# Optimization experiments

Hardware: AMD Instinct MI355X
Metric: run time of the kernel (lower is better)

## Reference

```python
import jax, jax.numpy as jnp
import numpy as np

N_NODES = 50000
N_EDGES = 800000
N_GRAPHS = 64
FEAT = 32      # bbox node features
EMB = 32       # category embedding dim
HID = 128      # hidden_feature_dim
OUT = 256      # out_feature_dim
NCAT = 1496    # category vocab (from nn.Embedding(1496, emb))


def setup_inputs() -> dict:
    key = jax.random.key(0)
    ks = jax.random.split(key, 24)
    s = lambda *sh: 1.0 / np.sqrt(sh[0])
    inp = {
        'nodes': jax.random.normal(ks[0], (N_NODES, FEAT), dtype=jnp.float32),
        'node_categories': jax.random.randint(ks[1], (N_NODES,), 0, NCAT),
        'edge_index': jax.random.randint(ks[2], (2, N_EDGES), 0, N_NODES),
        'batch': jnp.sort(jax.random.randint(ks[3], (N_NODES,), 0, N_GRAPHS)),
        'cat_emb': jax.random.normal(ks[4], (NCAT, EMB), dtype=jnp.float32),
        # GCNConv weights (x @ W + b)
        'W1': jax.random.normal(ks[5], (FEAT + EMB, HID), dtype=jnp.float32) * s(FEAT + EMB),
        'b1': jnp.zeros((HID,), jnp.float32),
        'W2': jax.random.normal(ks[6], (HID, HID), dtype=jnp.float32) * s(HID),
        'b2': jnp.zeros((HID,), jnp.float32),
        'W3': jax.random.normal(ks[7], (HID, HID), dtype=jnp.float32) * s(HID),
        'b3': jnp.zeros((HID,), jnp.float32),
        # EdgeConv MLP: Linear(2H,H) -> ReLU -> Linear(H,H)
        'We1': jax.random.normal(ks[8], (2 * HID, HID), dtype=jnp.float32) * s(2 * HID),
        'be1': jnp.zeros((HID,), jnp.float32),
        'We2': jax.random.normal(ks[9], (HID, HID), dtype=jnp.float32) * s(HID),
        'be2': jnp.zeros((HID,), jnp.float32),
        # head MLP
        'Wf1': jax.random.normal(ks[10], (2 * HID, OUT), dtype=jnp.float32) * s(2 * HID),
        'bf1': jnp.zeros((OUT,), jnp.float32),
        'Wf2': jax.random.normal(ks[11], (OUT, OUT), dtype=jnp.float32) * s(OUT),
        'bf2': jnp.zeros((OUT,), jnp.float32),
    }
    return inp


def _gcn_conv(x, W, b, src, dst, norm, n):
    # GCNConv: D^{-1/2}(A+I)D^{-1/2} X W + b  (self loops included in src/dst)
    h = x @ W
    agg = jax.ops.segment_sum(h[src] * norm[:, None], dst, num_segments=n)
    return agg + b


def reference(nodes, node_categories, edge_index, batch, cat_emb,
              W1, b1, W2, b2, W3, b3, We1, be1, We2, be2,
              Wf1, bf1, Wf2, bf2):
    n = nodes.shape[0]
    src, dst = edge_index[0], edge_index[1]
    loop = jnp.arange(n)
    src_f = jnp.concatenate([src, loop])
    dst_f = jnp.concatenate([dst, loop])
    deg = jax.ops.segment_sum(jnp.ones_like(dst_f, dtype=jnp.float32), dst_f, num_segments=n)
    dinv = jax.lax.rsqrt(deg)  # deg >= 1 due to self loops
    norm = dinv[src_f] * dinv[dst_f]

    x = jnp.concatenate([nodes, cat_emb[node_categories]], axis=1)
    x = jax.nn.relu(_gcn_conv(x, W1, b1, src_f, dst_f, norm, n))
    x = jax.nn.relu(_gcn_conv(x, W2, b2, src_f, dst_f, norm, n))
    x = jax.nn.relu(_gcn_conv(x, W3, b3, src_f, dst_f, norm, n))

    # EdgeConv: max_j MLP([x_i, x_j - x_i]) over incoming edges (PyG convention)
    xi = x[dst]
    xj = x[src]
    m = jnp.concatenate([xi, xj - xi], axis=1)            # [E, 2H]
    m = jax.nn.relu(m @ We1 + be1) @ We2 + be2            # [E, H]
    agg = jax.ops.segment_max(m, dst, num_segments=n)
    agg = jnp.where(jnp.isfinite(agg), agg, 0.0)          # isolated nodes -> 0
    x = jax.nn.relu(agg)

    # global max pool || global mean pool per graph
    gmax = jax.ops.segment_max(x, batch, num_segments=N_GRAPHS)
    gmax = jnp.where(jnp.isfinite(gmax), gmax, 0.0)
    cnt = jax.ops.segment_sum(jnp.ones((n,), jnp.float32), batch, num_segments=N_GRAPHS)
    gsum = jax.ops.segment_sum(x, batch, num_segments=N_GRAPHS)
    gavg = gsum / jnp.maximum(cnt, 1.0)[:, None]
    g = jnp.concatenate([gmax, gavg], axis=1)             # [G, 2H]

    # dropout layers are identity in eval mode
    g = jax.nn.relu(g @ Wf1 + bf1)
    g = jax.nn.relu(g @ Wf2 + bf2)
    return g
```

## Files before the change

### kernel.cpp

```cpp
#include <hip/hip_runtime.h>

#define FEAT 32
#define EMB 32
#define HID 128
#define NGRAPHS 64

typedef short short8 __attribute__((ext_vector_type(8)));
typedef float f32x4 __attribute__((ext_vector_type(4)));

union B8 { uint4 q; unsigned u[4]; short8 v; };

__device__ __forceinline__ unsigned bf16_rne_bits(float f) {
  unsigned u = __float_as_uint(f);
  unsigned r = u + 0x7FFFu + ((u >> 16) & 1u);
  return r & 0xFFFF0000u;
}
__device__ __forceinline__ void split2(float a, float b, unsigned& hp, unsigned& lp) {
  unsigned ha = bf16_rne_bits(a), hb = bf16_rne_bits(b);
  float la = a - __uint_as_float(ha), lb = b - __uint_as_float(hb);
  unsigned laa = bf16_rne_bits(la), lbb = bf16_rne_bits(lb);
  hp = (ha >> 16) | (hb & 0xFFFF0000u);
  lp = (laa >> 16) | (lbb & 0xFFFF0000u);
}

__global__ void hist_k(const int* __restrict__ dst, int* __restrict__ indeg, int E) {
  int e = blockIdx.x * blockDim.x + threadIdx.x;
  if (e < E) atomicAdd(&indeg[dst[e]], 1);
}

__global__ void dinv_k(const int* __restrict__ indeg, float* __restrict__ dinv, int N) {
  int i = blockIdx.x * blockDim.x + threadIdx.x;
  if (i < N) dinv[i] = rsqrtf((float)indeg[i] + 1.0f);
}

__global__ __launch_bounds__(1024) void scanA_k(const int* __restrict__ indeg,
                                                int* __restrict__ excl,
                                                int* __restrict__ bsum, int N) {
  __shared__ int wsum[16];
  int i = blockIdx.x * 1024 + threadIdx.x;
  const int lane = threadIdx.x & 63;
  const int wid = threadIdx.x >> 6;
  int val = (i < N) ? indeg[i] : 0;
  int x = val;
#pragma unroll
  for (int off = 1; off < 64; off <<= 1) {
    int y = __shfl_up(x, off, 64);
    if (lane >= off) x += y;
  }
  if (lane == 63) wsum[wid] = x;
  __syncthreads();
  if (wid == 0) {
    int s = (lane < 16) ? wsum[lane] : 0;
#pragma unroll
    for (int off = 1; off < 16; off <<= 1) {
      int y = __shfl_up(s, off, 64);
      if (lane >= off) s += y;
    }
    if (lane < 16) wsum[lane] = s;
  }
  __syncthreads();
  int ex = x - val + ((wid > 0) ? wsum[wid - 1] : 0);
  if (i < N) excl[i] = ex;
  if (threadIdx.x == 0) bsum[blockIdx.x] = wsum[15];
}

__global__ void scanB_k(int* __restrict__ bsum, int nb) {
  int lane = threadIdx.x;
  int v = (lane < nb) ? bsum[lane] : 0;
  int x = v;
#pragma unroll
  for (int off = 1; off < 64; off <<= 1) {
    int y = __shfl_up(x, off, 64);
    if (lane >= off) x += y;
  }
  if (lane < nb) bsum[lane] = x - v;
  if (lane == nb - 1) bsum[nb] = x;
}

__global__ __launch_bounds__(1024) void scanC_k(const int* __restrict__ excl,
                                                const int* __restrict__ bsum,
                                                int* __restrict__ row_start,
                                                int* __restrict__ cursor, int N, int nb) {
  int i = blockIdx.x * 1024 + threadIdx.x;
  if (i < N) {
    int v = excl[i] + bsum[blockIdx.x];
    row_start[i] = v;
    cursor[i] = v;
  }
  if (i == 0) row_start[N] = bsum[nb];
}

__global__ void fill_k(const int* __restrict__ src, const int* __restrict__ dst,
                       const float* __restrict__ dinv, int* __restrict__ cursor,
                       int* __restrict__ csr_src, int* __restrict__ csr_dst,
                       float* __restrict__ csr_norm, int E) {
  int e = blockIdx.x * blockDim.x + threadIdx.x;
  if (e >= E) return;
  int d = dst[e], s = src[e];
  int p = atomicAdd(&cursor[d], 1);
  csr_src[p] = s;
  csr_dst[p] = d;
  csr_norm[p] = dinv[s] * dinv[d];
}

__global__ void pack_k(const float* __restrict__ WA, const float* __restrict__ WB,
                       unsigned short* __restrict__ out, int K) {
  int t = blockIdx.x * blockDim.x + threadIdx.x;
  if (t >= K * 128) return;
  int k = t >> 7, c = t & 127;
  float v = WA[k * 128 + c];
  if (WB) v -= WB[k * 128 + c];
  unsigned hb = bf16_rne_bits(v);
  float lo = v - __uint_as_float(hb);
  unsigned lb = bf16_rne_bits(lo);
  int kt = k >> 5, ks = (k >> 3) & 3, j = k & 7;
  int idx = ((kt * 4 + ks) * 128 + c) * 8 + j;
  out[idx] = (unsigned short)(hb >> 16);
  out[K * 128 + idx] = (unsigned short)(lb >> 16);
}

__global__ void xcat_split_k(const float* __restrict__ nodes, const int* __restrict__ cats,
                             const float* __restrict__ emb, unsigned* __restrict__ xh,
                             unsigned* __restrict__ xl, int N) {
  int t = blockIdx.x * blockDim.x + threadIdx.x;
  if (t >= N * 32) return;
  int i = t >> 5, p = t & 31;
  float2 v = (p < 16) ? ((const float2*)nodes)[(size_t)i * 16 + p]
                      : ((const float2*)emb)[(size_t)cats[i] * 16 + (p - 16)];
  unsigned hp, lp;
  split2(v.x, v.y, hp, lp);
  xh[(size_t)i * 32 + p] = hp;
  xl[(size_t)i * 32 + p] = lp;
}

__global__ __launch_bounds__(256) void gemm_mfma(const unsigned short* __restrict__ Ah,
                                                 const unsigned short* __restrict__ Al,
                                                 const unsigned short* __restrict__ Bp,
                                                 float* __restrict__ C, int M, int K) {
  __shared__ uint4 Blds[4096];
  const int nq = K * 32;
  for (int i = threadIdx.x; i < nq; i += 256) Blds[i] = ((const uint4*)Bp)[i];
  __syncthreads();
  const int w = threadIdx.x >> 6, lane = threadIdx.x & 63;
  const int ks = lane >> 4, fr = lane & 15;
  const int rb0 = blockIdx.x * 128 + w * 32;
  const int loBase = K * 16;
  f32x4 acc[2][8];
#pragma unroll
  for (int m = 0; m < 2; ++m)
#pragma unroll
    for (int ct = 0; ct < 8; ++ct) acc[m][ct] = (f32x4)0.f;

  const int nkt = K >> 5;
  for (int kt = 0; kt < nkt; ++kt) {
    B8 ah[2], al[2];
#pragma unroll
    for (int m = 0; m < 2; ++m) {
      size_t off = (size_t)(rb0 + m * 16 + fr) * K + kt * 32 + ks * 8;
      ah[m].q = *(const uint4*)(Ah + off);
      al[m].q = *(const uint4*)(Al + off);
    }
#pragma unroll
    for (int ct = 0; ct < 8; ++ct) {
      int bidx = (kt * 4 + ks) * 128 + ct * 16 + fr;
      B8 bh, bl;
      bh.q = Blds[bidx];
      bl.q = Blds[bidx + loBase];
#pragma unroll
      for (int m = 0; m < 2; ++m) {
        acc[m][ct] = __builtin_amdgcn_mfma_f32_16x16x32_bf16(ah[m].v, bh.v, acc[m][ct], 0, 0, 0);
        acc[m][ct] = __builtin_amdgcn_mfma_f32_16x16x32_bf16(ah[m].v, bl.v, acc[m][ct], 0, 0, 0);
        acc[m][ct] = __builtin_amdgcn_mfma_f32_16x16x32_bf16(al[m].v, bh.v, acc[m][ct], 0, 0, 0);
      }
    }
  }
#pragma unroll
  for (int m = 0; m < 2; ++m)
#pragma unroll
    for (int ct = 0; ct < 8; ++ct) {
      int col = ct * 16 + fr;
#pragma unroll
      for (int r = 0; r < 4; ++r) {
        int row = rb0 + m * 16 + ks * 4 + r;
        if (row < M) C[(size_t)row * 128 + col] = acc[m][ct][r];
      }
    }
}

__global__ __launch_bounds__(256) void gemm_dual_mfma(const unsigned short* __restrict__ Ah,
                                                      const unsigned short* __restrict__ Al,
                                                      const unsigned short* __restrict__ Bp1,
                                                      const unsigned short* __restrict__ Bp2,
                                                      const float* __restrict__ bias1,
                                                      float* __restrict__ U,
                                                      float* __restrict__ V, int M) {
  __shared__ uint4 Blds[4096];
  for (int i = threadIdx.x; i < 4096; i += 256) Blds[i] = ((const uint4*)Bp1)[i];
  const int w = threadIdx.x >> 6, lane = threadIdx.x & 63;
  const int ks = lane >> 4, fr = lane & 15;
  const int rb0 = blockIdx.x * 128 + w * 32;
  B8 ah[2][4], al[2][4];
#pragma unroll
  for (int m = 0; m < 2; ++m)
#pragma unroll
    for (int kt = 0; kt < 4; ++kt) {
      size_t off = (size_t)(rb0 + m * 16 + fr) * 128 + kt * 32 + ks * 8;
      ah[m][kt].q = *(const uint4*)(Ah + off);
      al[m][kt].q = *(const uint4*)(Al + off);
    }
  __syncthreads();

  f32x4 acc[2][8];
#pragma unroll
  for (int m = 0; m < 2; ++m)
#pragma unroll
    for (int ct = 0; ct < 8; ++ct) acc[m][ct] = (f32x4)0.f;
#pragma unroll
  for (int kt = 0; kt < 4; ++kt)
#pragma unroll
    for (int ct = 0; ct < 8; ++ct) {
      int bidx = (kt * 4 + ks) * 128 + ct * 16 + fr;
      B8 bh, bl;
      bh.q = Blds[bidx];
      bl.q = Blds[bidx + 2048];
#pragma unroll
      for (int m = 0; m < 2; ++m) {
        acc[m][ct] = __builtin_amdgcn_mfma_f32_16x16x32_bf16(ah[m][kt].v, bh.v, acc[m][ct], 0, 0, 0);
        acc[m][ct] = __builtin_amdgcn_mfma_f32_16x16x32_bf16(ah[m][kt].v, bl.v, acc[m][ct], 0, 0, 0);
        acc[m][ct] = __builtin_amdgcn_mfma_f32_16x16x32_bf16(al[m][kt].v, bh.v, acc[m][ct], 0, 0, 0);
      }
    }
#pragma unroll
  for (int m = 0; m < 2; ++m)
#pragma unroll
    for (int ct = 0; ct < 8; ++ct) {
      int col = ct * 16 + fr;
      float bv = bias1[col];
#pragma unroll
      for (int r = 0; r < 4; ++r) {
        int row = rb0 + m * 16 + ks * 4 + r;
        if (row < M) U[(size_t)row * 128 + col] = acc[m][ct][r] + bv;
      }
    }

  __syncthreads();
  for (int i = threadIdx.x; i < 4096; i += 256) Blds[i] = ((const uint4*)Bp2)[i];
  __syncthreads();

#pragma unroll
  for (int m = 0; m < 2; ++m)
#pragma unroll
    for (int ct = 0; ct < 8; ++ct) acc[m][ct] = (f32x4)0.f;
#pragma unroll
  for (int kt = 0; kt < 4; ++kt)
#pragma unroll
    for (int ct = 0; ct < 8; ++ct) {
      int bidx = (kt * 4 + ks) * 128 + ct * 16 + fr;
      B8 bh, bl;
      bh.q = Blds[bidx];
      bl.q = Blds[bidx + 2048];
#pragma unroll
      for (int m = 0; m < 2; ++m) {
        acc[m][ct] = __builtin_amdgcn_mfma_f32_16x16x32_bf16(ah[m][kt].v, bh.v, acc[m][ct], 0, 0, 0);
        acc[m][ct] = __builtin_amdgcn_mfma_f32_16x16x32_bf16(ah[m][kt].v, bl.v, acc[m][ct], 0, 0, 0);
        acc[m][ct] = __builtin_amdgcn_mfma_f32_16x16x32_bf16(al[m][kt].v, bh.v, acc[m][ct], 0, 0, 0);
      }
    }
#pragma unroll
  for (int m = 0; m < 2; ++m)
#pragma unroll
    for (int ct = 0; ct < 8; ++ct) {
      int col = ct * 16 + fr;
#pragma unroll
      for (int r = 0; r < 4; ++r) {
        int row = rb0 + m * 16 + ks * 4 + r;
        if (row < M) V[(size_t)row * 128 + col] = acc[m][ct][r];
      }
    }
}

__global__ __launch_bounds__(256) void gcn_agg_split_k(
    const float* __restrict__ h, const int* __restrict__ csr_src,
    const float* __restrict__ csr_norm, const int* __restrict__ row_start,
    const float* __restrict__ dinv, const float* __restrict__ bias,
    unsigned* __restrict__ out_hi, unsigned* __restrict__ out_lo, int N) {
  int i = (blockIdx.x * blockDim.x + threadIdx.x) >> 6;
  int lane = threadIdx.x & 63;
  if (i >= N) return;
  const int g = lane >> 4, c8 = (lane & 15) * 8;
  float4 a0 = make_float4(0.f, 0.f, 0.f, 0.f);
  float4 a1 = make_float4(0.f, 0.f, 0.f, 0.f);
  int s0 = row_start[i], s1 = row_start[i + 1];
  if (g == 0) {
    float di = dinv[i];
    float sn = di * di;
    float4 v0 = *(const float4*)&h[(size_t)i * 128 + c8];
    float4 v1 = *(const float4*)&h[(size_t)i * 128 + c8 + 4];
    a0.x = v0.x * sn; a0.y = v0.y * sn; a0.z = v0.z * sn; a0.w = v0.w * sn;
    a1.x = v1.x * sn; a1.y = v1.y * sn; a1.z = v1.z * sn; a1.w = v1.w * sn;
  }
  for (int p = s0 + g; p < s1; p += 16) {
    int idx[4]; float wt[4];
#pragma unroll
    for (int j = 0; j < 4; ++j) {
      int q = p + 4 * j;
      if (q < s1) { idx[j] = csr_src[q]; wt[j] = csr_norm[q]; }
      else        { idx[j] = 0;          wt[j] = 0.f; }
    }
#pragma unroll
    for (int j = 0; j < 4; ++j) {
      const float4* hp = (const float4*)&h[(size_t)idx[j] * 128 + c8];
      float4 h0 = hp[0], h1 = hp[1];
      float wgt = wt[j];
      a0.x = fmaf(h0.x, wgt, a0.x); a0.y = fmaf(h0.y, wgt, a0.y);
      a0.z = fmaf(h0.z, wgt, a0.z); a0.w = fmaf(h0.w, wgt, a0.w);
      a1.x = fmaf(h1.x, wgt, a1.x); a1.y = fmaf(h1.y, wgt, a1.y);
      a1.z = fmaf(h1.z, wgt, a1.z); a1.w = fmaf(h1.w, wgt, a1.w);
    }
  }
#pragma unroll
  for (int off = 16; off < 64; off <<= 1) {
    a0.x += __shfl_xor(a0.x, off); a0.y += __shfl_xor(a0.y, off);
    a0.z += __shfl_xor(a0.z, off); a0.w += __shfl_xor(a0.w, off);
    a1.x += __shfl_xor(a1.x, off); a1.y += __shfl_xor(a1.y, off);
    a1.z += __shfl_xor(a1.z, off); a1.w += __shfl_xor(a1.w, off);
  }
  if (g == 0) {
    float4 b0 = *(const float4*)&bias[c8];
    float4 b1 = *(const float4*)&bias[c8 + 4];
    float v0 = fmaxf(a0.x + b0.x, 0.f), v1 = fmaxf(a0.y + b0.y, 0.f);
    float v2 = fmaxf(a0.z + b0.z, 0.f), v3 = fmaxf(a0.w + b0.w, 0.f);
    float v4 = fmaxf(a1.x + b1.x, 0.f), v5 = fmaxf(a1.y + b1.y, 0.f);
    float v6 = fmaxf(a1.z + b1.z, 0.f), v7 = fmaxf(a1.w + b1.w, 0.f);
    uint4 hh, ll;
    split2(v0, v1, hh.x, ll.x);
    split2(v2, v3, hh.y, ll.y);
    split2(v4, v5, hh.z, ll.z);
    split2(v6, v7, hh.w, ll.w);
    *(uint4*)&out_hi[(size_t)i * 64 + (lane & 15) * 4] = hh;
    *(uint4*)&out_lo[(size_t)i * 64 + (lane & 15) * 4] = ll;
  }
}

__global__ __launch_bounds__(256) void edgeconv_mfma(
    const float* __restrict__ U, const float* __restrict__ V,
    const int* __restrict__ csr_src, const int* __restrict__ csr_dst,
    const unsigned short* __restrict__ We2p, const float* __restrict__ be2,
    unsigned* __restrict__ agg, int E, int ntiles) {
  __shared__ uint4 Blds[4096];
  for (int i = threadIdx.x; i < 4096; i += 256) Blds[i] = ((const uint4*)We2p)[i];
  __syncthreads();
  const int w = threadIdx.x >> 6, lane = threadIdx.x & 63;
  const int ks = lane >> 4, fr = lane & 15;
  float b2[8];
#pragma unroll
  for (int ct = 0; ct < 8; ++ct) b2[ct] = be2[ct * 16 + fr];

  auto loadIdx = [&](int t, int (&d)[2], int (&s)[2]) {
    const int eb = t * 128 + w * 32;
#pragma unroll
    for (int m = 0; m < 2; ++m) {
      int el = ((fr >> 2) << 3) + (m << 2) + (fr & 3);
      int e = eb + el;
      int ee = (e < E) ? e : 0;
      d[m] = csr_dst[ee];
      s[m] = csr_src[ee];
    }
  };

  int tile = blockIdx.x;
  int dA[2] = {0, 0}, sA[2] = {0, 0};
  float4 ru[2][2][2], rv[2][2][2];
  if (tile < ntiles) {
    loadIdx(tile, dA, sA);
    const int k0 = ks * 8;
#pragma unroll
    for (int m = 0; m < 2; ++m) {
      const float4* up = (const float4*)&U[(size_t)dA[m] * 128 + k0];
      const float4* vp = (const float4*)&V[(size_t)sA[m] * 128 + k0];
      ru[0][m][0] = up[0]; ru[0][m][1] = up[1];
      rv[0][m][0] = vp[0]; rv[0][m][1] = vp[1];
    }
  }

  for (; tile < ntiles; tile += gridDim.x) {
    const int eb = tile * 128 + w * 32;
    int dN[2] = {0, 0}, sN[2] = {0, 0};
    const int tn = tile + gridDim.x;
    if (tn < ntiles) loadIdx(tn, dN, sN);

    f32x4 acc[2][8];
#pragma unroll
    for (int m = 0; m < 2; ++m)
#pragma unroll
      for (int ct = 0; ct < 8; ++ct) acc[m][ct] = (f32x4)0.f;

#pragma unroll
    for (int kt = 0; kt < 4; ++kt) {
      const int cb = kt & 1, nb = cb ^ 1;
      if (kt < 3) {
        const int k0n = (kt + 1) * 32 + ks * 8;
#pragma unroll
        for (int m = 0; m < 2; ++m) {
          const float4* up = (const float4*)&U[(size_t)dA[m] * 128 + k0n];
          const float4* vp = (const float4*)&V[(size_t)sA[m] * 128 + k0n];
          ru[nb][m][0] = up[0]; ru[nb][m][1] = up[1];
          rv[nb][m][0] = vp[0]; rv[nb][m][1] = vp[1];
        }
      } else {
        const int k0n = ks * 8;
#pragma unroll
        for (int m = 0; m < 2; ++m) {
          const float4* up = (const float4*)&U[(size_t)dN[m] * 128 + k0n];
          const float4* vp = (const float4*)&V[(size_t)sN[m] * 128 + k0n];
          ru[0][m][0] = up[0]; ru[0][m][1] = up[1];
          rv[0][m][0] = vp[0]; rv[0][m][1] = vp[1];
        }
      }
      B8 ah[2], al[2];
#pragma unroll
      for (int m = 0; m < 2; ++m) {
        float4 u0 = ru[cb][m][0], u1 = ru[cb][m][1];
        float4 v0 = rv[cb][m][0], v1 = rv[cb][m][1];
        float s0 = fmaxf(u0.x + v0.x, 0.f);
        float s1 = fmaxf(u0.y + v0.y, 0.f);
        float s2 = fmaxf(u0.z + v0.z, 0.f);
        float s3 = fmaxf(u0.w + v0.w, 0.f);
        float s4 = fmaxf(u1.x + v1.x, 0.f);
        float s5 = fmaxf(u1.y + v1.y, 0.f);
        float s6 = fmaxf(u1.z + v1.z, 0.f);
        float s7 = fmaxf(u1.w + v1.w, 0.f);
        split2(s0, s1, ah[m].u[0], al[m].u[0]);
        split2(s2, s3, ah[m].u[1], al[m].u[1]);
        split2(s4, s5, ah[m].u[2], al[m].u[2]);
        split2(s6, s7, ah[m].u[3], al[m].u[3]);
      }
      __builtin_amdgcn_s_setprio(1);
#pragma unroll
      for (int ct = 0; ct < 8; ++ct) {
        int bidx = (kt * 4 + ks) * 128 + ct * 16 + fr;
        B8 bh, bl;
        bh.q = Blds[bidx];
        bl.q = Blds[bidx + 2048];
#pragma unroll
        for (int m = 0; m < 2; ++m) {
          acc[m][ct] = __builtin_amdgcn_mfma_f32_16x16x32_bf16(ah[m].v, bh.v, acc[m][ct], 0, 0, 0);
          acc[m][ct] = __builtin_amdgcn_mfma_f32_16x16x32_bf16(ah[m].v, bl.v, acc[m][ct], 0, 0, 0);
          acc[m][ct] = __builtin_amdgcn_mfma_f32_16x16x32_bf16(al[m].v, bh.v, acc[m][ct], 0, 0, 0);
        }
      }
      __builtin_amdgcn_s_setprio(0);
    }
    const int ebase = eb + ks * 8;
    int prev = -1;
    float runv[8];
#pragma unroll
    for (int j = 0; j < 8; ++j) {
      int e = ebase + j;
      if (e < E) {
        int d = csr_dst[e];
        const int m = j >> 2, r = j & 3;
        if (d != prev) {
          if (prev >= 0) {
#pragma unroll
            for (int ct = 0; ct < 8; ++ct)
              atomicMax(&agg[(size_t)prev * 128 + ct * 16 + fr], __float_as_uint(runv[ct]));
          }
          prev = d;
#pragma unroll
          for (int ct = 0; ct < 8; ++ct) runv[ct] = fmaxf(acc[m][ct][r] + b2[ct], 0.f);
        } else {
#pragma unroll
          for (int ct = 0; ct < 8; ++ct)
            runv[ct] = fmaxf(runv[ct], fmaxf(acc[m][ct][r] + b2[ct], 0.f));
        }
      }
    }
    if (prev >= 0) {
#pragma unroll
      for (int ct = 0; ct < 8; ++ct)
        atomicMax(&agg[(size_t)prev * 128 + ct * 16 + fr], __float_as_uint(runv[ct]));
    }
    dA[0] = dN[0]; dA[1] = dN[1];
    sA[0] = sN[0]; sA[1] = sN[1];
  }
}

__global__ void gbound_k(const int* __restrict__ batch, int* __restrict__ gstart, int N) {
  int g = threadIdx.x;
  if (g > NGRAPHS) return;
  if (g == NGRAPHS) { gstart[NGRAPHS] = N; return; }
  int lo = 0, hi = N;
  while (lo < hi) {
    int mid = (lo + hi) >> 1;
    if (batch[mid] < g) lo = mid + 1; else hi = mid;
  }
  gstart[g] = lo;
}

__global__ __launch_bounds__(256) void pool_seg_k(const float* __restrict__ x,
                                                  const int* __restrict__ gstart,
                                                  unsigned* __restrict__ gmax,
                                                  float* __restrict__ gsum) {
  int g = blockIdx.x >> 3, s = blockIdx.x & 7;
  int lb = gstart[g], ub = gstart[g + 1];
  long len = ub - lb;
  int i0 = lb + (int)((len * s) >> 3);
  int i1 = lb + (int)((len * (s + 1)) >> 3);
  int c = threadIdx.x & 127, h = threadIdx.x >> 7;
  float m = 0.f, sm = 0.f;
  for (int i = i0 + h; i < i1; i += 2) {
    float v = x[(size_t)i * 128 + c];
    m = fmaxf(m, v);
    sm += v;
  }
  if (i1 > i0) {
    atomicMax(&gmax[g * 128 + c], __float_as_uint(m));
    atomicAdd(&gsum[g * 128 + c], sm);
  }
}

__global__ void g0_k(const unsigned* __restrict__ gmax, const float* __restrict__ gsum,
                     const int* __restrict__ gstart, float* __restrict__ g0) {
  int t = blockIdx.x * blockDim.x + threadIdx.x;
  int g = t >> 8, c = t & 255;
  float o;
  if (c < 128) o = __uint_as_float(gmax[g * 128 + c]);
  else {
    float cnt = (float)(gstart[g + 1] - gstart[g]);
    o = gsum[g * 128 + (c - 128)] / fmaxf(cnt, 1.f);
  }
  g0[t] = o;
}

__global__ __launch_bounds__(256) void fc_k(const float* __restrict__ X,
                                            const float* __restrict__ W,
                                            const float* __restrict__ b,
                                            float* __restrict__ Y, int K, int N) {
  __shared__ float xs[256];
  int g = blockIdx.x, c = threadIdx.x;
  for (int k = c; k < K; k += blockDim.x) xs[k] = X[g * K + k];
  __syncthreads();
  float acc = b[c];
  for (int k = 0; k < K; k++) acc = fmaf(xs[k], W[(size_t)k * N + c], acc);
  Y[g * N + c] = fmaxf(acc, 0.f);
}

extern "C" void kernel_launch(void* const* d_in, const int* in_sizes, int n_in,
                              void* d_out, int out_size, void* d_ws, size_t ws_size,
                              hipStream_t stream) {
  const float* nodes = (const float*)d_in[0];
  const int* cats = (const int*)d_in[1];
  const int* eidx = (const int*)d_in[2];
  const int* batch = (const int*)d_in[3];
  const float* emb = (const float*)d_in[4];
  const float* W1 = (const float*)d_in[5];
  const float* b1 = (const float*)d_in[6];
  const float* W2 = (const float*)d_in[7];
  const float* b2 = (const float*)d_in[8];
  const float* W3 = (const float*)d_in[9];
  const float* b3 = (const float*)d_in[10];
  const float* We1 = (const float*)d_in[11];
  const float* be1 = (const float*)d_in[12];
  const float* We2 = (const float*)d_in[13];
  const float* be2 = (const float*)d_in[14];
  const float* Wf1 = (const float*)d_in[15];
  const float* bf1 = (const float*)d_in[16];
  const float* Wf2 = (const float*)d_in[17];
  const float* bf2 = (const float*)d_in[18];
  float* out = (float*)d_out;

  const int N = in_sizes[0] / FEAT;
  const int E = in_sizes[2] / 2;
  const int Npad = ((N + 127) / 128) * 128;
  const int* src = eidx;
  const int* dst = eidx + E;

  char* w = (char*)d_ws;
  auto alloc = [&](size_t bytes) -> void* {
    void* p = (void*)w;
    w += (bytes + 255) & ~(size_t)255;
    return p;
  };
  unsigned* xh = (unsigned*)alloc((size_t)Npad * 32 * 4);
  unsigned* xl = (unsigned*)alloc((size_t)Npad * 32 * 4);
  unsigned* ahb = (unsigned*)alloc((size_t)Npad * 64 * 4);
  unsigned* alb = (unsigned*)alloc((size_t)Npad * 64 * 4);
  float* bufF = (float*)alloc((size_t)Npad * 128 * 4);
  float* bufV = (float*)alloc((size_t)Npad * 128 * 4);
  unsigned* agg = (unsigned*)alloc((size_t)N * 128 * 4);
  int* indeg = (int*)alloc((size_t)N * 4);
  int* rowst = (int*)alloc((size_t)(N + 1) * 4);
  int* cursor = (int*)alloc((size_t)N * 4);
  int* exclb = (int*)alloc((size_t)N * 4);
  int* bsum = (int*)alloc(128 * 4);
  float* dinv = (float*)alloc((size_t)N * 4);
  int* csr_src = (int*)alloc((size_t)E * 4);
  int* csr_dst = (int*)alloc((size_t)E * 4);
  float* csr_norm = (float*)alloc((size_t)E * 4);
  unsigned short* W1p = (unsigned short*)alloc(2 * 64 * 128 * 2);
  unsigned short* W2p = (unsigned short*)alloc(2 * 128 * 128 * 2);
  unsigned short* W3p = (unsigned short*)alloc(2 * 128 * 128 * 2);
  unsigned short* Wdp = (unsigned short*)alloc(2 * 128 * 128 * 2);
  unsigned short* Wvp = (unsigned short*)alloc(2 * 128 * 128 * 2);
  unsigned short* We2p = (unsigned short*)alloc(2 * 128 * 128 * 2);
  float* g0buf = (float*)alloc(NGRAPHS * 256 * 4);
  float* g1buf = (float*)alloc(NGRAPHS * 256 * 4);
  unsigned* gmax = (unsigned*)alloc(NGRAPHS * 128 * 4);
  float* gsum = (float*)alloc(NGRAPHS * 128 * 4);
  int* gstart = (int*)alloc((NGRAPHS + 1) * 4);
  if ((size_t)(w - (char*)d_ws) > ws_size) return;

  hipMemsetAsync(indeg, 0, (size_t)N * 4, stream);
  hipMemsetAsync(agg, 0, (size_t)N * 128 * 4, stream);
  hipMemsetAsync(gmax, 0, NGRAPHS * 128 * 4, stream);
  hipMemsetAsync(gsum, 0, NGRAPHS * 128 * 4, stream);

  const int TB = 256;
  int gE = (E + TB - 1) / TB;
  int gN = (N + TB - 1) / TB;
  int nb = (N + 1023) / 1024;

  hist_k<<<gE, TB, 0, stream>>>(dst, indeg, E);
  dinv_k<<<gN, TB, 0, stream>>>(indeg, dinv, N);
  scanA_k<<<nb, 1024, 0, stream>>>(indeg, exclb, bsum, N);
  scanB_k<<<1, 64, 0, stream>>>(bsum, nb);
  scanC_k<<<nb, 1024, 0, stream>>>(exclb, bsum, rowst, cursor, N, nb);
  fill_k<<<gE, TB, 0, stream>>>(src, dst, dinv, cursor, csr_src, csr_dst, csr_norm, E);
  gbound_k<<<1, 128, 0, stream>>>(batch, gstart, N);

  xcat_split_k<<<(N * 32 + TB - 1) / TB, TB, 0, stream>>>(nodes, cats, emb, xh, xl, N);

  pack_k<<<32, TB, 0, stream>>>(W1, nullptr, W1p, 64);
  pack_k<<<64, TB, 0, stream>>>(W2, nullptr, W2p, 128);
  pack_k<<<64, TB, 0, stream>>>(W3, nullptr, W3p, 128);
  pack_k<<<64, TB, 0, stream>>>(We1, We1 + 128 * 128, Wdp, 128);
  pack_k<<<64, TB, 0, stream>>>(We1 + 128 * 128, nullptr, Wvp, 128);
  pack_k<<<64, TB, 0, stream>>>(We2, nullptr, We2p, 128);

  const int gemmGrid = Npad / 128;
  const int waveGrid = (N * 64 + TB - 1) / TB;

  gemm_mfma<<<gemmGrid, TB, 0, stream>>>((unsigned short*)xh, (unsigned short*)xl, W1p, bufF, N, 64);
  gcn_agg_split_k<<<waveGrid, TB, 0, stream>>>(bufF, csr_src, csr_norm, rowst, dinv, b1, ahb, alb, N);
  gemm_mfma<<<gemmGrid, TB, 0, stream>>>((unsigned short*)ahb, (unsigned short*)alb, W2p, bufF, N, 128);
  gcn_agg_split_k<<<waveGrid, TB, 0, stream>>>(bufF, csr_src, csr_norm, rowst, dinv, b2, ahb, alb, N);
  gemm_mfma<<<gemmGrid, TB, 0, stream>>>((unsigned short*)ahb, (unsigned short*)alb, W3p, bufF, N, 128);
  gcn_agg_split_k<<<waveGrid, TB, 0, stream>>>(bufF, csr_src, csr_norm, rowst, dinv, b3, ahb, alb, N);

  gemm_dual_mfma<<<gemmGrid, TB, 0, stream>>>((unsigned short*)ahb, (unsigned short*)alb,
                                              Wdp, Wvp, be1, bufF, bufV, N);

  const int ntiles = (E + 127) / 128;
  edgeconv_mfma<<<2048, TB, 0, stream>>>(bufF, bufV, csr_src, csr_dst, We2p, be2, agg, E, ntiles);

  pool_seg_k<<<NGRAPHS * 8, TB, 0, stream>>>((const float*)agg, gstart, gmax, gsum);
  g0_k<<<NGRAPHS, TB, 0, stream>>>(gmax, gsum, gstart, g0buf);
  fc_k<<<NGRAPHS, 256, 0, stream>>>(g0buf, Wf1, bf1, g1buf, 256, 256);
  fc_k<<<NGRAPHS, 256, 0, stream>>>(g1buf, Wf2, bf2, out, 256, 256);
}
```

Before: 708.0 us.

## Aggregate first layer before GEMM and fuse small setup kernels

```diff
diff --git a/kernel.cpp b/kernel.cpp
--- a/kernel.cpp
+++ b/kernel.cpp
@@ -28,19 +28,16 @@
   if (e < E) atomicAdd(&indeg[dst[e]], 1);
 }
 
-__global__ void dinv_k(const int* __restrict__ indeg, float* __restrict__ dinv, int N) {
-  int i = blockIdx.x * blockDim.x + threadIdx.x;
-  if (i < N) dinv[i] = rsqrtf((float)indeg[i] + 1.0f);
-}
-
 __global__ __launch_bounds__(1024) void scanA_k(const int* __restrict__ indeg,
                                                 int* __restrict__ excl,
-                                                int* __restrict__ bsum, int N) {
+                                                int* __restrict__ bsum,
+                                                float* __restrict__ dinv, int N) {
   __shared__ int wsum[16];
   int i = blockIdx.x * 1024 + threadIdx.x;
   const int lane = threadIdx.x & 63;
   const int wid = threadIdx.x >> 6;
   int val = (i < N) ? indeg[i] : 0;
+  if (i < N) dinv[i] = rsqrtf((float)val + 1.0f);
   int x = val;
 #pragma unroll
   for (int off = 1; off < 64; off <<= 1) {
@@ -103,9 +100,24 @@
   csr_norm[p] = dinv[s] * dinv[d];
 }
 
-__global__ void pack_k(const float* __restrict__ WA, const float* __restrict__ WB,
-                       unsigned short* __restrict__ out, int K) {
-  int t = blockIdx.x * blockDim.x + threadIdx.x;
+__global__ void pack_all_k(const float* __restrict__ W1, const float* __restrict__ W2,
+                           const float* __restrict__ W3, const float* __restrict__ We1,
+                           const float* __restrict__ We2,
+                           unsigned short* __restrict__ W1p, unsigned short* __restrict__ W2p,
+                           unsigned short* __restrict__ W3p, unsigned short* __restrict__ Wdp,
+                           unsigned short* __restrict__ Wvp, unsigned short* __restrict__ We2p) {
+  int b = blockIdx.x;
+  const float* WA;
+  const float* WB = nullptr;
+  unsigned short* out;
+  int K, t0;
+  if (b < 32)       { WA = W1;            out = W1p;  K = 64;  t0 = b; }
+  else if (b < 96)  { WA = W2;            out = W2p;  K = 128; t0 = b - 32; }
+  else if (b < 160) { WA = W3;            out = W3p;  K = 128; t0 = b - 96; }
+  else if (b < 224) { WA = We1; WB = We1 + 16384; out = Wdp; K = 128; t0 = b - 160; }
+  else if (b < 288) { WA = We1 + 16384;   out = Wvp;  K = 128; t0 = b - 224; }
+  else              { WA = We2;           out = We2p; K = 128; t0 = b - 288; }
+  int t = t0 * 256 + threadIdx.x;
   if (t >= K * 128) return;
   int k = t >> 7, c = t & 127;
   float v = WA[k * 128 + c];
@@ -131,6 +143,67 @@
   split2(v.x, v.y, hp, lp);
   xh[(size_t)i * 32 + p] = hp;
   xl[(size_t)i * 32 + p] = lp;
+}
+
+__global__ __launch_bounds__(256) void gcn_aggpre_k(
+    const unsigned* __restrict__ xh, const unsigned* __restrict__ xl,
+    const int* __restrict__ csr_src, const float* __restrict__ csr_norm,
+    const int* __restrict__ row_start, const float* __restrict__ dinv,
+    unsigned* __restrict__ out_hi, unsigned* __restrict__ out_lo, int N) {
+  int i = (blockIdx.x * blockDim.x + threadIdx.x) >> 6;
+  int lane = threadIdx.x & 63;
+  if (i >= N) return;
+  const int g = lane >> 5, cp = lane & 31;
+  float a0 = 0.f, a1 = 0.f;
+  int s0 = row_start[i], s1 = row_start[i + 1];
+  if (g == 0) {
+    float di = dinv[i];
+    float sn = di * di;
+    unsigned uh = xh[(size_t)i * 32 + cp], ul = xl[(size_t)i * 32 + cp];
+    float x0 = __uint_as_float(uh << 16) + __uint_as_float(ul << 16);
+    float x1 = __uint_as_float(uh & 0xFFFF0000u) + __uint_as_float(ul & 0xFFFF0000u);
+    a0 = x0 * sn;
+    a1 = x1 * sn;
+  }
+  for (int p = s0 + g; p < s1; p += 8) {
+    int idx[4]; float wt[4];
+#pragma unroll
+    for (int j = 0; j < 4; ++j) {
+      int q = p + 2 * j;
+      if (q < s1) { idx[j] = csr_src[q]; wt[j] = csr_norm[q]; }
+      else        { idx[j] = 0;          wt[j] = 0.f; }
+    }
+#pragma unroll
+    for (int j = 0; j < 4; ++j) {
+      unsigned uh = xh[(size_t)idx[j] * 32 + cp], ul = xl[(size_t)idx[j] * 32 + cp];
+      float x0 = __uint_as_float(uh << 16) + __uint_as_float(ul << 16);
+      float x1 = __uint_as_float(uh & 0xFFFF0000u) + __uint_as_float(ul & 0xFFFF0000u);
+      a0 = fmaf(x0, wt[j], a0);
+      a1 = fmaf(x1, wt[j], a1);
+    }
+  }
+  a0 += __shfl_xor(a0, 32);
+  a1 += __shfl_xor(a1, 32);
+  if (g == 0) {
+    unsigned hp, lp;
+    split2(a0, a1, hp, lp);
+    out_hi[(size_t)i * 32 + cp] = hp;
+    out_lo[(size_t)i * 32 + cp] = lp;
+  }
+}
+
+__global__ void brs_k(const float* __restrict__ h, const float* __restrict__ bias,
+                      unsigned* __restrict__ out_hi, unsigned* __restrict__ out_lo, int N) {
+  int t = blockIdx.x * blockDim.x + threadIdx.x;
+  if (t >= N * 64) return;
+  int i = t >> 6, p = t & 63;
+  float2 v = ((const float2*)h)[(size_t)i * 64 + p];
+  float2 bv = ((const float2*)bias)[p];
+  float a0 = fmaxf(v.x + bv.x, 0.f), a1 = fmaxf(v.y + bv.y, 0.f);
+  unsigned hp, lp;
+  split2(a0, a1, hp, lp);
+  out_hi[(size_t)i * 64 + p] = hp;
+  out_lo[(size_t)i * 64 + p] = lp;
 }
 
 __global__ __launch_bounds__(256) void gemm_mfma(const unsigned short* __restrict__ Ah,
@@ -520,17 +593,25 @@
   }
 }
 
-__global__ void g0_k(const unsigned* __restrict__ gmax, const float* __restrict__ gsum,
-                     const int* __restrict__ gstart, float* __restrict__ g0) {
-  int t = blockIdx.x * blockDim.x + threadIdx.x;
-  int g = t >> 8, c = t & 255;
-  float o;
-  if (c < 128) o = __uint_as_float(gmax[g * 128 + c]);
+__global__ __launch_bounds__(256) void fc1_k(const unsigned* __restrict__ gmax,
+                                             const float* __restrict__ gsum,
+                                             const int* __restrict__ gstart,
+                                             const float* __restrict__ W,
+                                             const float* __restrict__ b,
+                                             float* __restrict__ Y) {
+  __shared__ float xs[256];
+  int g = blockIdx.x, c = threadIdx.x;
+  float xv;
+  if (c < 128) xv = __uint_as_float(gmax[g * 128 + c]);
   else {
     float cnt = (float)(gstart[g + 1] - gstart[g]);
-    o = gsum[g * 128 + (c - 128)] / fmaxf(cnt, 1.f);
-  }
-  g0[t] = o;
+    xv = gsum[g * 128 + (c - 128)] / fmaxf(cnt, 1.f);
+  }
+  xs[c] = xv;
+  __syncthreads();
+  float acc = b[c];
+  for (int k = 0; k < 256; k++) acc = fmaf(xs[k], W[(size_t)k * 256 + c], acc);
+  Y[g * 256 + c] = fmaxf(acc, 0.f);
 }
 
 __global__ __launch_bounds__(256) void fc_k(const float* __restrict__ X,
@@ -584,6 +665,8 @@
   };
   unsigned* xh = (unsigned*)alloc((size_t)Npad * 32 * 4);
   unsigned* xl = (unsigned*)alloc((size_t)Npad * 32 * 4);
+  unsigned* aggh = (unsigned*)alloc((size_t)Npad * 32 * 4);
+  unsigned* aggl = (unsigned*)alloc((size_t)Npad * 32 * 4);
   unsigned* ahb = (unsigned*)alloc((size_t)Npad * 64 * 4);
   unsigned* alb = (unsigned*)alloc((size_t)Npad * 64 * 4);
   float* bufF = (float*)alloc((size_t)Npad * 128 * 4);
@@ -604,7 +687,6 @@
   unsigned short* Wdp = (unsigned short*)alloc(2 * 128 * 128 * 2);
   unsigned short* Wvp = (unsigned short*)alloc(2 * 128 * 128 * 2);
   unsigned short* We2p = (unsigned short*)alloc(2 * 128 * 128 * 2);
-  float* g0buf = (float*)alloc(NGRAPHS * 256 * 4);
   float* g1buf = (float*)alloc(NGRAPHS * 256 * 4);
   unsigned* gmax = (unsigned*)alloc(NGRAPHS * 128 * 4);
   float* gsum = (float*)alloc(NGRAPHS * 128 * 4);
@@ -618,31 +700,24 @@
 
   const int TB = 256;
   int gE = (E + TB - 1) / TB;
-  int gN = (N + TB - 1) / TB;
   int nb = (N + 1023) / 1024;
 
   hist_k<<<gE, TB, 0, stream>>>(dst, indeg, E);
-  dinv_k<<<gN, TB, 0, stream>>>(indeg, dinv, N);
-  scanA_k<<<nb, 1024, 0, stream>>>(indeg, exclb, bsum, N);
+  scanA_k<<<nb, 1024, 0, stream>>>(indeg, exclb, bsum, dinv, N);
   scanB_k<<<1, 64, 0, stream>>>(bsum, nb);
   scanC_k<<<nb, 1024, 0, stream>>>(exclb, bsum, rowst, cursor, N, nb);
   fill_k<<<gE, TB, 0, stream>>>(src, dst, dinv, cursor, csr_src, csr_dst, csr_norm, E);
   gbound_k<<<1, 128, 0, stream>>>(batch, gstart, N);
 
   xcat_split_k<<<(N * 32 + TB - 1) / TB, TB, 0, stream>>>(nodes, cats, emb, xh, xl, N);
-
-  pack_k<<<32, TB, 0, stream>>>(W1, nullptr, W1p, 64);
-  pack_k<<<64, TB, 0, stream>>>(W2, nullptr, W2p, 128);
-  pack_k<<<64, TB, 0, stream>>>(W3, nullptr, W3p, 128);
-  pack_k<<<64, TB, 0, stream>>>(We1, We1 + 128 * 128, Wdp, 128);
-  pack_k<<<64, TB, 0, stream>>>(We1 + 128 * 128, nullptr, Wvp, 128);
-  pack_k<<<64, TB, 0, stream>>>(We2, nullptr, We2p, 128);
+  pack_all_k<<<352, TB, 0, stream>>>(W1, W2, W3, We1, We2, W1p, W2p, W3p, Wdp, Wvp, We2p);
 
   const int gemmGrid = Npad / 128;
   const int waveGrid = (N * 64 + TB - 1) / TB;
 
-  gemm_mfma<<<gemmGrid, TB, 0, stream>>>((unsigned short*)xh, (unsigned short*)xl, W1p, bufF, N, 64);
-  gcn_agg_split_k<<<waveGrid, TB, 0, stream>>>(bufF, csr_src, csr_norm, rowst, dinv, b1, ahb, alb, N);
+  gcn_aggpre_k<<<waveGrid, TB, 0, stream>>>(xh, xl, csr_src, csr_norm, rowst, dinv, aggh, aggl, N);
+  gemm_mfma<<<gemmGrid, TB, 0, stream>>>((unsigned short*)aggh, (unsigned short*)aggl, W1p, bufF, N, 64);
+  brs_k<<<(N * 64 + TB - 1) / TB, TB, 0, stream>>>(bufF, b1, ahb, alb, N);
   gemm_mfma<<<gemmGrid, TB, 0, stream>>>((unsigned short*)ahb, (unsigned short*)alb, W2p, bufF, N, 128);
   gcn_agg_split_k<<<waveGrid, TB, 0, stream>>>(bufF, csr_src, csr_norm, rowst, dinv, b2, ahb, alb, N);
   gemm_mfma<<<gemmGrid, TB, 0, stream>>>((unsigned short*)ahb, (unsigned short*)alb, W3p, bufF, N, 128);
@@ -655,7 +730,6 @@
   edgeconv_mfma<<<2048, TB, 0, stream>>>(bufF, bufV, csr_src, csr_dst, We2p, be2, agg, E, ntiles);
 
   pool_seg_k<<<NGRAPHS * 8, TB, 0, stream>>>((const float*)agg, gstart, gmax, gsum);
-  g0_k<<<NGRAPHS, TB, 0, stream>>>(gmax, gsum, gstart, g0buf);
-  fc_k<<<NGRAPHS, 256, 0, stream>>>(g0buf, Wf1, bf1, g1buf, 256, 256);
+  fc1_k<<<NGRAPHS, 256, 0, stream>>>(gmax, gsum, gstart, Wf1, bf1, g1buf);
   fc_k<<<NGRAPHS, 256, 0, stream>>>(g1buf, Wf2, bf2, out, 256, 256);
 }
```

After: 662.7 us. 1.07x faster.
